# Kernel tuning notes

Measured on AMD Instinct MI355X. Metric: run time of the kernel, lower is better.

Reference implementation:

```python
import jax, jax.numpy as jnp
import numpy as np

DIM = 1024
HEADS = 16
DIM_HEAD = 64
INNER = HEADS * DIM_HEAD  # 1024
SCALE = DIM_HEAD ** -0.5


def setup_inputs() -> dict:
    key = jax.random.key(0)
    k1, k2, k3, k4 = jax.random.split(key, 4)
    x = jax.random.normal(k1, (2, 2048, DIM), dtype=jnp.float32)
    # nn.Linear(dim, inner*3, bias=False): weight [3*inner, dim]; store transposed [dim, 3*inner]
    w_qkv = jax.random.normal(k2, (DIM, 3 * INNER), dtype=jnp.float32) * (DIM ** -0.5)
    w_out = jax.random.normal(k3, (INNER, DIM), dtype=jnp.float32) * (INNER ** -0.5)
    b_out = jax.random.normal(k4, (DIM,), dtype=jnp.float32) * 0.02
    return {"x": x, "w_qkv": w_qkv, "w_out": w_out, "b_out": b_out}


def _attention(x, w_qkv, w_out, b_out):
    b, n, _ = x.shape
    qkv = x @ w_qkv  # [b, n, 3*inner]
    q_chunk = qkv[..., :INNER]  # NOTE: source bug — q, k, v all come from chunk 0
    def split_heads(t):
        return t.reshape(b, n, HEADS, DIM_HEAD).transpose(0, 2, 1, 3)  # b h n d
    q = split_heads(q_chunk) * SCALE
    k = split_heads(q_chunk)
    v = split_heads(q_chunk)
    dots = jnp.einsum('bhid,bhjd->bhij', q, k)
    mask_value = -jnp.finfo(dots.dtype).max
    causal_mask = jnp.triu(jnp.ones((n, n), dtype=bool), k=1)
    dots = jnp.where(causal_mask, mask_value, dots)
    attn = jax.nn.softmax(dots, axis=-1)
    out = jnp.einsum('bhij,bhjd->bhid', attn, v)
    out = out.transpose(0, 2, 1, 3).reshape(b, n, INNER)
    return out @ w_out + b_out


def reference(x, w_qkv, w_out, b_out):
    return _attention(x, w_qkv, w_out, b_out)
```

## Files before the change

### kernel.cpp

```cpp
#include <hip/hip_runtime.h>
#include <hip/hip_bf16.h>

typedef __attribute__((ext_vector_type(8))) short short8;
typedef __attribute__((ext_vector_type(4))) short bf16x4;
typedef __attribute__((ext_vector_type(4))) float floatx4;

#define MFMA16(a, b, c) __builtin_amdgcn_mfma_f32_16x16x32_bf16((a), (b), (c), 0, 0, 0)

#if defined(__HIP_DEVICE_COMPILE__)
  #if __has_builtin(__builtin_amdgcn_mfma_f32_16x16x16bf16_1k)
    #define MFMA_PV(a, b, c) __builtin_amdgcn_mfma_f32_16x16x16bf16_1k((a), (b), (c), 0, 0, 0)
  #elif __has_builtin(__builtin_amdgcn_mfma_f32_16x16x16_bf16)
    #define MFMA_PV(a, b, c) __builtin_amdgcn_mfma_f32_16x16x16_bf16((a), (b), (c), 0, 0, 0)
  #else
    #error "no 16x16x16 bf16 MFMA builtin found on device pass"
  #endif
#else
  #define MFMA_PV(a, b, c) (c)
#endif

#if defined(__HIP_DEVICE_COMPILE__) && __has_builtin(__builtin_amdgcn_global_load_lds)
  #define HAVE_GLOAD 1
#else
  #define HAVE_GLOAD 0
#endif

__device__ __forceinline__ void gload16(const void* g, void* l) {
#if HAVE_GLOAD
    __builtin_amdgcn_global_load_lds(
        (const __attribute__((address_space(1))) void*)g,
        (__attribute__((address_space(3))) void*)l, 16, 0, 0);
#else
    (void)g; (void)l;
#endif
}

#define SEQ    2048
#define DIMM   1024
#define HEADS  16
#define DHEAD  64
#define ROWS   4096
#define K1 0.18033688011112043f
#define K2 (-34.62468098133512f)

__global__ void cvt_bf16_kernel(const float* __restrict__ src,
                                __hip_bfloat16* __restrict__ dst) {
    const size_t i = (size_t)(blockIdx.x * 256 + threadIdx.x) * 4;
    floatx4 v = *(const floatx4*)(src + i);
    union { bf16x4 s; __hip_bfloat16 h[4]; } u;
#pragma unroll
    for (int j = 0; j < 4; j++) u.h[j] = __float2bfloat16(v[j]);
    *(bf16x4*)(dst + i) = u.s;
}

__global__ __launch_bounds__(256) void transpose_cvt2_kernel(
    const float* __restrict__ W1, __hip_bfloat16* __restrict__ WT1,
    const float* __restrict__ W2, __hip_bfloat16* __restrict__ WT2) {
    __shared__ __hip_bfloat16 tile[64][72];
    const float* W        = blockIdx.z ? W2 : W1;
    __hip_bfloat16* WT    = blockIdx.z ? WT2 : WT1;
    const int ld          = blockIdx.z ? DIMM : 3 * DIMM;
    const int tid = threadIdx.x;
    const int r = tid >> 2, c0 = (tid & 3) * 16;
    const int k0 = blockIdx.x * 64;
    const int n0 = blockIdx.y * 64;
    const float* src = W + (size_t)(k0 + r) * ld + n0 + c0;
    union { short8 v; __hip_bfloat16 h[8]; } a0, a1;
#pragma unroll
    for (int j = 0; j < 8; j++) {
        a0.h[j] = __float2bfloat16(src[j]);
        a1.h[j] = __float2bfloat16(src[8 + j]);
    }
    *(short8*)&tile[r][c0]     = a0.v;
    *(short8*)&tile[r][c0 + 8] = a1.v;
    __syncthreads();
    union { short8 v; __hip_bfloat16 h[8]; } u0, u1;
#pragma unroll
    for (int j = 0; j < 8; j++) {
        u0.h[j] = tile[c0 + j][r];
        u1.h[j] = tile[c0 + 8 + j][r];
    }
    __hip_bfloat16* dst = WT + (size_t)(n0 + r) * 1024 + k0 + c0;
    *(short8*)dst       = u0.v;
    *(short8*)(dst + 8) = u1.v;
}

__global__ __launch_bounds__(256) void transpose_t_kernel(
    const __hip_bfloat16* __restrict__ t,
    __hip_bfloat16* __restrict__ Tt) {
    __shared__ __hip_bfloat16 tile[64][72];
    const int tid = threadIdx.x;
    const int r = tid >> 2, c0 = (tid & 3) * 16;
    const int row0 = blockIdx.x * 64;
    const int col0 = blockIdx.y * 64;
    const __hip_bfloat16* src = t + (size_t)(row0 + r) * DIMM + col0 + c0;
    *(short8*)&tile[r][c0]     = *(const short8*)src;
    *(short8*)&tile[r][c0 + 8] = *(const short8*)(src + 8);
    __syncthreads();
    const int cb = (c0 >> 4) * 4;
    union { short8 v; __hip_bfloat16 h[8]; } u0, u1;
#pragma unroll
    for (int j = 0; j < 8; j++) {
        u0.h[j] = tile[(j >> 2) * 16 + cb + (j & 3)][r];
        u1.h[j] = tile[((j >> 2) + 2) * 16 + cb + (j & 3)][r];
    }
    __hip_bfloat16* dst = Tt + (size_t)(col0 + r) * ROWS + row0 + c0;
    *(short8*)dst       = u0.v;
    *(short8*)(dst + 8) = u1.v;
}

template <typename CT>
__global__ __launch_bounds__(256) void gemm_bf_kernel(
    const __hip_bfloat16* __restrict__ A,
    const __hip_bfloat16* __restrict__ BT,
    const float* __restrict__ bias,
    CT* __restrict__ C, int M, int N, int K) {
    __shared__ __align__(16) __hip_bfloat16 As[2][64][64];
    __shared__ __align__(16) __hip_bfloat16 Bs[2][64][64];

    const int tid  = threadIdx.x;
    const int lane = tid & 63, wid = tid >> 6;
    const int wm   = wid >> 1, wn = wid & 1;
    const int quad = lane >> 4, l15 = lane & 15;
    const int bm = blockIdx.y * 64, bn = blockIdx.x * 64;

    floatx4 acc[2][2];
#pragma unroll
    for (int r = 0; r < 2; r++)
#pragma unroll
        for (int c = 0; c < 2; c++) acc[r][c] = (floatx4){0.f, 0.f, 0.f, 0.f};

    const int g_row = wid * 8 + (lane >> 3);
    const int g_col = (((lane & 7) ^ (lane >> 3)) << 3);
    const int ldst  = (wid << 10);

    auto stage = [&](int k0, int buf) {
#if HAVE_GLOAD
#pragma unroll
        for (int j = 0; j < 2; j++) {
            gload16(A + (size_t)(bm + j * 32 + g_row) * K + k0 + g_col,
                    (char*)&As[buf][0][0] + j * 4096 + ldst);
            gload16(BT + (size_t)(bn + j * 32 + g_row) * K + k0 + g_col,
                    (char*)&Bs[buf][0][0] + j * 4096 + ldst);
        }
#else
#pragma unroll
        for (int j = 0; j < 2; j++) {
            short8 va = *(const short8*)(A + (size_t)(bm + j * 32 + g_row) * K + k0 + g_col);
            *(short8*)((char*)&As[buf][0][0] + j * 4096 + ldst + ((lane & 63) << 4)) = va;
            short8 vb = *(const short8*)(BT + (size_t)(bn + j * 32 + g_row) * K + k0 + g_col);
            *(short8*)((char*)&Bs[buf][0][0] + j * 4096 + ldst + ((lane & 63) << 4)) = vb;
        }
#endif
    };

    stage(0, 0);
    __syncthreads();

    const int hq = l15 & 7;
    const int nk = K >> 6;
    for (int kb = 0; kb < nk; ++kb) {
        const int buf = kb & 1;
        if (kb + 1 < nk) stage((kb + 1) << 6, buf ^ 1);
#pragma unroll
        for (int ks = 0; ks < 2; ks++) {
            const int col = (((ks << 2) + quad) ^ hq) << 3;
            short8 af[2], bfr[2];
#pragma unroll
            for (int r = 0; r < 2; r++)
                af[r] = *(const short8*)&As[buf][wm * 32 + r * 16 + l15][col];
#pragma unroll
            for (int c = 0; c < 2; c++)
                bfr[c] = *(const short8*)&Bs[buf][wn * 32 + c * 16 + l15][col];
#pragma unroll
            for (int r = 0; r < 2; r++)
#pragma unroll
                for (int c = 0; c < 2; c++)
                    acc[r][c] = MFMA16(af[r], bfr[c], acc[r][c]);
        }
        __syncthreads();
    }

#pragma unroll
    for (int c = 0; c < 2; c++) {
        const int col = bn + wn * 32 + c * 16 + l15;
        const float bv = bias ? bias[col] : 0.f;
#pragma unroll
        for (int r = 0; r < 2; r++) {
            const int row0 = bm + wm * 32 + r * 16 + quad * 4;
#pragma unroll
            for (int i = 0; i < 4; i++) {
                const float v = acc[r][c][i] + bv;
                if constexpr (__is_same(CT, float))
                    C[(size_t)(row0 + i) * N + col] = v;
                else
                    C[(size_t)(row0 + i) * N + col] = __float2bfloat16(v);
            }
        }
    }
}

template <typename AT, typename CT>
__global__ __launch_bounds__(256) void gemm_fp_kernel(
    const AT* __restrict__ A, const float* __restrict__ B,
    const float* __restrict__ bias, CT* __restrict__ C,
    int M, int N, int K, int ldb) {
    __shared__ __align__(16) __hip_bfloat16 As[2][64][40];
    __shared__ __align__(16) __hip_bfloat16 Bs[2][128][40];
    const int tid = threadIdx.x;
    const int lane = tid & 63, wid = tid >> 6;
    const int wm = wid >> 1, wn = wid & 1;
    const int quad = lane >> 4, l15 = lane & 15;
    const int bm = blockIdx.y * 64, bn = blockIdx.x * 128;
    floatx4 acc[2][4];
#pragma unroll
    for (int r = 0; r < 2; r++)
#pragma unroll
        for (int c = 0; c < 4; c++) acc[r][c] = (floatx4){0.f, 0.f, 0.f, 0.f};
    const int a_lr = tid >> 2, a_lc = (tid & 3) * 8;
    const int b_kr = tid & 31, b_nc = (tid >> 5) * 16;
    floatx4 raf0, raf1; short8 rab; floatx4 rb[4];
    auto load_tile = [&](int k0) {
        const AT* pa = A + (size_t)(bm + a_lr) * K + k0 + a_lc;
        if constexpr (__is_same(AT, float)) {
            raf0 = *(const floatx4*)pa; raf1 = *(const floatx4*)(pa + 4);
        } else { rab = *(const short8*)pa; }
        const float* pb = B + (size_t)(k0 + b_kr) * ldb + bn + b_nc;
#pragma unroll
        for (int q = 0; q < 4; q++) rb[q] = *(const floatx4*)(pb + 4 * q);
    };
    auto store_tile = [&](int buf) {
        if constexpr (__is_same(AT, float)) {
            __align__(16) __hip_bfloat16 hh[8];
#pragma unroll
            for (int j = 0; j < 4; j++) {
                hh[j] = __float2bfloat16(raf0[j]); hh[4 + j] = __float2bfloat16(raf1[j]);
            }
            *(short8*)&As[buf][a_lr][a_lc] = *(short8*)&hh[0];
        } else { *(short8*)&As[buf][a_lr][a_lc] = rab; }
#pragma unroll
        for (int q = 0; q < 4; q++)
#pragma unroll
            for (int j = 0; j < 4; j++)
                Bs[buf][b_nc + 4 * q + j][b_kr] = __float2bfloat16(rb[q][j]);
    };
    load_tile(0); store_tile(0);
    if (K > 32) load_tile(32);
    __syncthreads();
    const int nk = K >> 5;
    for (int kb = 0; kb < nk; ++kb) {
        const int buf = kb & 1;
        short8 af[2], bf[4];
#pragma unroll
        for (int r = 0; r < 2; r++)
            af[r] = *(const short8*)&As[buf][wm * 32 + r * 16 + l15][quad * 8];
#pragma unroll
        for (int c = 0; c < 4; c++)
            bf[c] = *(const short8*)&Bs[buf][wn * 64 + c * 16 + l15][quad * 8];
#pragma unroll
        for (int r = 0; r < 2; r++)
#pragma unroll
            for (int c = 0; c < 4; c++)
                acc[r][c] = MFMA16(af[r], bf[c], acc[r][c]);
        if (kb + 1 < nk) store_tile(buf ^ 1);
        if (kb + 2 < nk) load_tile((kb + 2) << 5);
        __syncthreads();
    }
#pragma unroll
    for (int c = 0; c < 4; c++) {
        const int col = bn + wn * 64 + c * 16 + l15;
        const float bv = bias ? bias[col] : 0.f;
#pragma unroll
        for (int r = 0; r < 2; r++) {
            const int row0 = bm + wm * 32 + r * 16 + quad * 4;
#pragma unroll
            for (int i = 0; i < 4; i++) {
                const float v = acc[r][c][i] + bv;
                if constexpr (__is_same(CT, float)) C[(size_t)(row0 + i) * N + col] = v;
                else C[(size_t)(row0 + i) * N + col] = __float2bfloat16(v);
            }
        }
    }
}

__global__ __launch_bounds__(256) void attn_kernel(
    const __hip_bfloat16* __restrict__ T,
    const __hip_bfloat16* __restrict__ Tt,
    __hip_bfloat16* __restrict__ O) {
    __shared__ __align__(16) __hip_bfloat16 Ks[2][64][72];
    __shared__ __align__(16) __hip_bfloat16 Vt[2][64][72];

    const int tid  = threadIdx.x;
    const int lane = tid & 63, wid = tid >> 6;
    const int quad = lane >> 4, l15 = lane & 15;

    const int bx = blockIdx.x;
    const int half = bx >> 9, idx = bx & 511;
    const int g = idx & 15, h = (idx >> 4) & 15, b = idx >> 8;
    const int qt = half ? g : 31 - g;

    const size_t rowbase = (size_t)b * SEQ;
    const int hoff  = h * DHEAD;
    const int qrow0 = qt * 64;

    short8 qf[2];
    {
        const __hip_bfloat16* qp =
            T + (rowbase + qrow0 + wid * 16 + l15) * DIMM + hoff + quad * 8;
        qf[0] = *(const short8*)qp;
        qf[1] = *(const short8*)(qp + 32);
    }

    float l_lane = 0.f;
    floatx4 accO[4];
#pragma unroll
    for (int dt = 0; dt < 4; dt++) accO[dt] = (floatx4){0.f,0.f,0.f,0.f};

    const int sr = tid >> 2;
    const int sc = (tid & 3) * 16;

    short8 rK0, rK1, rV0, rV1;
    auto load_tile = [&](int kt) {
        const __hip_bfloat16* pK = T + (rowbase + kt * 64 + sr) * DIMM + hoff + sc;
        rK0 = *(const short8*)pK; rK1 = *(const short8*)(pK + 8);
        const __hip_bfloat16* pV =
            Tt + (size_t)(hoff + sr) * ROWS + rowbase + kt * 64 + sc;
        rV0 = *(const short8*)pV; rV1 = *(const short8*)(pV + 8);
    };
    auto store_tile = [&](int buf) {
        *(short8*)&Ks[buf][sr][sc]     = rK0;
        *(short8*)&Ks[buf][sr][sc + 8] = rK1;
        *(short8*)&Vt[buf][sr][sc]     = rV0;
        *(short8*)&Vt[buf][sr][sc + 8] = rV1;
    };

    const int last = qt;
    load_tile(0);
    store_tile(0);
    if (last >= 1) load_tile(1);
    __syncthreads();

    for (int kt = 0; kt <= last; ++kt) {
        const int buf = kt & 1;

        floatx4 s[4];
#pragma unroll
        for (int c = 0; c < 4; c++) {
            s[c] = (floatx4){0.f,0.f,0.f,0.f};
#pragma unroll
            for (int ks = 0; ks < 2; ks++) {
                short8 kfr = *(const short8*)&Ks[buf][c * 16 + l15][ks * 32 + quad * 8];
                s[c] = MFMA16(kfr, qf[ks], s[c]);
            }
        }

        bf16x4 pk[4];
        const bool need_mask = (kt == last);
#pragma unroll
        for (int c = 0; c < 4; c++) {
            union { bf16x4 v; __hip_bfloat16 hh[4]; } u;
            float sum = 0.f;
#pragma unroll
            for (int i = 0; i < 4; i++) {
                float v = exp2f(fmaf(s[c][i], K1, K2));
                if (need_mask) {
                    const int key  = kt * 64 + c * 16 + quad * 4 + i;
                    const int qrow = qrow0 + wid * 16 + l15;
                    if (key > qrow) v = 0.f;
                }
                sum += v;
                u.hh[i] = __float2bfloat16(v);
            }
            l_lane += sum;
            pk[c] = u.v;
        }

#pragma unroll
        for (int dt = 0; dt < 4; dt++) {
            union { short8 v; bf16x4 b[2]; } uv, uw;
            uv.v = *(const short8*)&Vt[buf][dt * 16 + l15][quad * 16];
            uw.v = *(const short8*)&Vt[buf][dt * 16 + l15][quad * 16 + 8];
            accO[dt] = MFMA_PV(pk[0], uv.b[0], accO[dt]);
            accO[dt] = MFMA_PV(pk[1], uv.b[1], accO[dt]);
            accO[dt] = MFMA_PV(pk[2], uw.b[0], accO[dt]);
            accO[dt] = MFMA_PV(pk[3], uw.b[1], accO[dt]);
        }

        if (kt < last)      store_tile(buf ^ 1);
        if (kt + 2 <= last) load_tile(kt + 2);
        __syncthreads();
    }

    l_lane += __shfl_xor(l_lane, 16);
    l_lane += __shfl_xor(l_lane, 32);
    float inv[4];
#pragma unroll
    for (int i = 0; i < 4; i++)
        inv[i] = 1.f / __shfl(l_lane, quad * 4 + i, 64);
#pragma unroll
    for (int dt = 0; dt < 4; dt++)
#pragma unroll
        for (int i = 0; i < 4; i++) {
            const size_t row = rowbase + qrow0 + wid * 16 + quad * 4 + i;
            O[row * DIMM + hoff + dt * 16 + l15] =
                __float2bfloat16(accO[dt][i] * inv[i]);
        }
}

extern "C" void kernel_launch(void* const* d_in, const int* in_sizes, int n_in,
                              void* d_out, int out_size, void* d_ws, size_t ws_size,
                              hipStream_t stream) {
    const float* x     = (const float*)d_in[0];
    const float* w_qkv = (const float*)d_in[1];
    const float* w_out = (const float*)d_in[2];
    const float* b_out = (const float*)d_in[3];
    float* out = (float*)d_out;

    __hip_bfloat16* t  = (__hip_bfloat16*)d_out;
    __hip_bfloat16* Tt = (__hip_bfloat16*)((char*)d_out + (8u << 20));
    char* ws = (char*)d_ws;
    __hip_bfloat16* ob = (__hip_bfloat16*)ws;

    if (ws_size >= (size_t)(20u << 20)) {
        __hip_bfloat16* xb  = (__hip_bfloat16*)(ws + (8u  << 20));
        __hip_bfloat16* w1t = (__hip_bfloat16*)(ws + (16u << 20));
        __hip_bfloat16* w2t = (__hip_bfloat16*)(ws + (18u << 20));

        cvt_bf16_kernel<<<4096, 256, 0, stream>>>(x, xb);
        transpose_cvt2_kernel<<<dim3(16, 16, 2), 256, 0, stream>>>(
            w_qkv, w1t, w_out, w2t);

        gemm_bf_kernel<__hip_bfloat16><<<dim3(16, 64), 256, 0, stream>>>(
            xb, w1t, nullptr, t, ROWS, DIMM, DIMM);
        transpose_t_kernel<<<dim3(64, 16), 256, 0, stream>>>(t, Tt);
        attn_kernel<<<dim3(1024), 256, 0, stream>>>(t, Tt, ob);
        gemm_bf_kernel<float><<<dim3(16, 64), 256, 0, stream>>>(
            ob, w2t, b_out, out, ROWS, DIMM, DIMM);
    } else {
        gemm_fp_kernel<float, __hip_bfloat16><<<dim3(8, 64), 256, 0, stream>>>(
            x, w_qkv, nullptr, t, ROWS, DIMM, DIMM, 3 * DIMM);
        transpose_t_kernel<<<dim3(64, 16), 256, 0, stream>>>(t, Tt);
        attn_kernel<<<dim3(1024), 256, 0, stream>>>(t, Tt, ob);
        gemm_fp_kernel<__hip_bfloat16, float><<<dim3(8, 64), 256, 0, stream>>>(
            ob, w_out, b_out, out, ROWS, DIMM, DIMM, DIMM);
    }
}
```

Measured before the change: 161.7 us.

## Fuse V transpose into QKV GEMM epilogue and async-stage K/V tiles in attention

The QKV GEMM now also writes a transposed bf16 copy of its output tile through shared memory, which removes the separate transpose kernel launch and its extra global read and write. The attention kernel replaces its register-staged K/V loading with direct global-to-LDS loads into XOR-swizzled unpadded tiles, prefetching the next tile during compute. This adds LDS traffic and a barrier to the GEMM epilogue, and relies on the swizzle to avoid bank conflicts now that the padding is gone.

```diff
diff --git a/kernel.cpp b/kernel.cpp
--- a/kernel.cpp
+++ b/kernel.cpp
@@ -114,7 +114,9 @@
     const __hip_bfloat16* __restrict__ A,
     const __hip_bfloat16* __restrict__ BT,
     const float* __restrict__ bias,
-    CT* __restrict__ C, int M, int N, int K) {
+    CT* __restrict__ C,
+    __hip_bfloat16* __restrict__ Tt,
+    int M, int N, int K) {
     __shared__ __align__(16) __hip_bfloat16 As[2][64][64];
     __shared__ __align__(16) __hip_bfloat16 Bs[2][64][64];
 
@@ -147,9 +149,9 @@
 #pragma unroll
         for (int j = 0; j < 2; j++) {
             short8 va = *(const short8*)(A + (size_t)(bm + j * 32 + g_row) * K + k0 + g_col);
-            *(short8*)((char*)&As[buf][0][0] + j * 4096 + ldst + ((lane & 63) << 4)) = va;
+            *(short8*)((char*)&As[buf][0][0] + j * 4096 + ldst + (lane << 4)) = va;
             short8 vb = *(const short8*)(BT + (size_t)(bn + j * 32 + g_row) * K + k0 + g_col);
-            *(short8*)((char*)&Bs[buf][0][0] + j * 4096 + ldst + ((lane & 63) << 4)) = vb;
+            *(short8*)((char*)&Bs[buf][0][0] + j * 4096 + ldst + (lane << 4)) = vb;
         }
 #endif
     };
@@ -197,6 +199,30 @@
                     C[(size_t)(row0 + i) * N + col] = __float2bfloat16(v);
             }
         }
+    }
+
+    if (Tt) {
+        __hip_bfloat16 (*tl)[68] = (__hip_bfloat16 (*)[68]) & As[0][0][0];
+#pragma unroll
+        for (int c = 0; c < 2; c++)
+#pragma unroll
+            for (int r = 0; r < 2; r++)
+#pragma unroll
+                for (int i = 0; i < 4; i++)
+                    tl[wm * 32 + r * 16 + quad * 4 + i][wn * 32 + c * 16 + l15] =
+                        __float2bfloat16(acc[r][c][i]);
+        __syncthreads();
+        const int rr = tid >> 2, cc0 = (tid & 3) * 16;
+        const int cb = (cc0 >> 4) * 4;
+        union { short8 v; __hip_bfloat16 h[8]; } u0, u1;
+#pragma unroll
+        for (int j = 0; j < 8; j++) {
+            u0.h[j] = tl[(j >> 2) * 16 + cb + (j & 3)][rr];
+            u1.h[j] = tl[((j >> 2) + 2) * 16 + cb + (j & 3)][rr];
+        }
+        __hip_bfloat16* dst = Tt + (size_t)(bn + rr) * ROWS + bm + cc0;
+        *(short8*)dst       = u0.v;
+        *(short8*)(dst + 8) = u1.v;
     }
 }
 
@@ -287,8 +313,8 @@
     const __hip_bfloat16* __restrict__ T,
     const __hip_bfloat16* __restrict__ Tt,
     __hip_bfloat16* __restrict__ O) {
-    __shared__ __align__(16) __hip_bfloat16 Ks[2][64][72];
-    __shared__ __align__(16) __hip_bfloat16 Vt[2][64][72];
+    __shared__ __align__(16) __hip_bfloat16 Ks[2][64][64];
+    __shared__ __align__(16) __hip_bfloat16 Vt[2][64][64];
 
     const int tid  = threadIdx.x;
     const int lane = tid & 63, wid = tid >> 6;
@@ -316,32 +342,38 @@
 #pragma unroll
     for (int dt = 0; dt < 4; dt++) accO[dt] = (floatx4){0.f,0.f,0.f,0.f};
 
-    const int sr = tid >> 2;
-    const int sc = (tid & 3) * 16;
-
-    short8 rK0, rK1, rV0, rV1;
-    auto load_tile = [&](int kt) {
-        const __hip_bfloat16* pK = T + (rowbase + kt * 64 + sr) * DIMM + hoff + sc;
-        rK0 = *(const short8*)pK; rK1 = *(const short8*)(pK + 8);
-        const __hip_bfloat16* pV =
-            Tt + (size_t)(hoff + sr) * ROWS + rowbase + kt * 64 + sc;
-        rV0 = *(const short8*)pV; rV1 = *(const short8*)(pV + 8);
+    const int g_row = wid * 8 + (lane >> 3);
+    const int g_col = (((lane & 7) ^ (lane >> 3)) << 3);
+    const int ldst  = (wid << 10);
+
+    auto stage = [&](int kt, int buf) {
+#if HAVE_GLOAD
+#pragma unroll
+        for (int j = 0; j < 2; j++) {
+            gload16(T + (rowbase + kt * 64 + j * 32 + g_row) * DIMM + hoff + g_col,
+                    (char*)&Ks[buf][0][0] + j * 4096 + ldst);
+            gload16(Tt + (size_t)(hoff + j * 32 + g_row) * ROWS + rowbase + kt * 64 + g_col,
+                    (char*)&Vt[buf][0][0] + j * 4096 + ldst);
+        }
+#else
+#pragma unroll
+        for (int j = 0; j < 2; j++) {
+            short8 vk = *(const short8*)(T + (rowbase + kt * 64 + j * 32 + g_row) * DIMM + hoff + g_col);
+            *(short8*)((char*)&Ks[buf][0][0] + j * 4096 + ldst + (lane << 4)) = vk;
+            short8 vv = *(const short8*)(Tt + (size_t)(hoff + j * 32 + g_row) * ROWS + rowbase + kt * 64 + g_col);
+            *(short8*)((char*)&Vt[buf][0][0] + j * 4096 + ldst + (lane << 4)) = vv;
+        }
+#endif
     };
-    auto store_tile = [&](int buf) {
-        *(short8*)&Ks[buf][sr][sc]     = rK0;
-        *(short8*)&Ks[buf][sr][sc + 8] = rK1;
-        *(short8*)&Vt[buf][sr][sc]     = rV0;
-        *(short8*)&Vt[buf][sr][sc + 8] = rV1;
-    };
 
     const int last = qt;
-    load_tile(0);
-    store_tile(0);
-    if (last >= 1) load_tile(1);
+    stage(0, 0);
     __syncthreads();
 
+    const int hq = l15 & 7;
     for (int kt = 0; kt <= last; ++kt) {
         const int buf = kt & 1;
+        if (kt + 1 <= last) stage(kt + 1, buf ^ 1);
 
         floatx4 s[4];
 #pragma unroll
@@ -349,7 +381,8 @@
             s[c] = (floatx4){0.f,0.f,0.f,0.f};
 #pragma unroll
             for (int ks = 0; ks < 2; ks++) {
-                short8 kfr = *(const short8*)&Ks[buf][c * 16 + l15][ks * 32 + quad * 8];
+                short8 kfr = *(const short8*)
+                    &Ks[buf][c * 16 + l15][(((ks << 2) + quad) ^ hq) << 3];
                 s[c] = MFMA16(kfr, qf[ks], s[c]);
             }
         }
@@ -378,16 +411,14 @@
 #pragma unroll
         for (int dt = 0; dt < 4; dt++) {
             union { short8 v; bf16x4 b[2]; } uv, uw;
-            uv.v = *(const short8*)&Vt[buf][dt * 16 + l15][quad * 16];
-            uw.v = *(const short8*)&Vt[buf][dt * 16 + l15][quad * 16 + 8];
+            uv.v = *(const short8*)&Vt[buf][dt * 16 + l15][((quad << 1) ^ hq) << 3];
+            uw.v = *(const short8*)&Vt[buf][dt * 16 + l15][(((quad << 1) | 1) ^ hq) << 3];
             accO[dt] = MFMA_PV(pk[0], uv.b[0], accO[dt]);
             accO[dt] = MFMA_PV(pk[1], uv.b[1], accO[dt]);
             accO[dt] = MFMA_PV(pk[2], uw.b[0], accO[dt]);
             accO[dt] = MFMA_PV(pk[3], uw.b[1], accO[dt]);
         }
 
-        if (kt < last)      store_tile(buf ^ 1);
-        if (kt + 2 <= last) load_tile(kt + 2);
         __syncthreads();
     }
 
@@ -431,11 +462,10 @@
             w_qkv, w1t, w_out, w2t);
 
         gemm_bf_kernel<__hip_bfloat16><<<dim3(16, 64), 256, 0, stream>>>(
-            xb, w1t, nullptr, t, ROWS, DIMM, DIMM);
-        transpose_t_kernel<<<dim3(64, 16), 256, 0, stream>>>(t, Tt);
+            xb, w1t, nullptr, t, Tt, ROWS, DIMM, DIMM);
         attn_kernel<<<dim3(1024), 256, 0, stream>>>(t, Tt, ob);
         gemm_bf_kernel<float><<<dim3(16, 64), 256, 0, stream>>>(
-            ob, w2t, b_out, out, ROWS, DIMM, DIMM);
+            ob, w2t, b_out, out, nullptr, ROWS, DIMM, DIMM);
     } else {
         gemm_fp_kernel<float, __hip_bfloat16><<<dim3(8, 64), 256, 0, stream>>>(
             x, w_qkv, nullptr, t, ROWS, DIMM, DIMM, 3 * DIMM);
```

Result: slower. 165.3 us (+2.2%).
